# Performance work log

Hardware: AMD Instinct MI355X
Metric: run time of the kernel (lower is better)

Reference implementation:

```python
import jax, jax.numpy as jnp
import numpy as np

N_X, N_U, N_Y = 256, 32, 32
BATCH, T = 16, 8192
LAM_MIN, LAM_MAX = 0.9, 0.995
B_SCALE, D_SCALE = 0.25, 0.25


def setup_inputs() -> dict:
    key = jax.random.key(0)
    k = jax.random.split(key, 6)
    # Orthogonal Q via QR of a random Gaussian matrix (as in the torch module)
    M = jax.random.normal(k[0], (N_X, N_X), dtype=jnp.float32)
    Q, _ = jnp.linalg.qr(M)
    lam = LAM_MIN + (LAM_MAX - LAM_MIN) * jax.random.uniform(k[1], (N_X,), dtype=jnp.float32)
    Bmat = B_SCALE * jax.random.normal(k[2], (N_X, N_U), dtype=jnp.float32)
    # C picks out the first n_y coordinates (C[i, i] = 1)
    C = jnp.eye(N_Y, N_X, dtype=jnp.float32)
    D = D_SCALE * jax.random.normal(k[3], (N_Y, N_U), dtype=jnp.float32)
    x0 = jax.random.normal(k[4], (BATCH, N_X), dtype=jnp.float32)
    u = jax.random.normal(k[5], (BATCH, T, N_U), dtype=jnp.float32)
    return {"x0": x0, "u": u, "Q": Q, "lam": lam, "Bmat": Bmat, "C": C, "D": D}


def _diag_scan(lam, v):
    """Diagonal linear recurrence x_t = lam * x_{t-1} + v_t (x_0 folded into v[:, 0]).

    lam: (N,), v: (B, T, N) -> states x_1..x_T of shape (B, T, N).
    """
    a = jnp.broadcast_to(lam, v.shape)

    def op(l, r):
        a1, b1 = l
        a2, b2 = r
        return a1 * a2, a2 * b1 + b2

    return jax.lax.associative_scan(op, (a, v), axis=1)[1]


def reference(x0, u, Q, lam, Bmat, C, D):
    Bz = Q.T @ Bmat            # (n_x, n_u) modal input matrix
    Cz = C @ Q                 # (n_y, n_x) modal output matrix
    z0 = x0 @ Q                # (B, n_x)   modal initial state
    v = jnp.einsum('btu,nu->btn', u, Bz)   # (B, T, n_x)
    v = v.at[:, 0].add(lam * z0)            # fold lam * z0 into first step
    z_next = _diag_scan(lam, v)             # (B, T, n_x) = z_1..z_T
    # y_t uses z_t for t = 0..T-1 (states[:, :-1] in the original)
    z_prev = jnp.concatenate([z0[:, None, :], z_next[:, :-1]], axis=1)
    y = jnp.einsum('btn,yn->bty', z_prev, Cz) + jnp.einsum('btu,yu->bty', u, D)
    return y
```

## Files before the change

### kernel.cpp

```cpp
#include <hip/hip_runtime.h>

typedef _Float16 half4_t __attribute__((ext_vector_type(4)));
typedef _Float16 half8_t __attribute__((ext_vector_type(8)));
typedef float f32x4 __attribute__((ext_vector_type(4)));

constexpr int NX = 256, NU = 32, NY = 32, BATCH = 16, T = 8192;
constexpr int NC = 64, L = 128;
constexpr int SUBT = 32, NSUB = L / SUBT;
constexpr int KW = NX + NU;
constexpr int ZP = 264;

__global__ __launch_bounds__(256) void k_pre(
    const float* __restrict__ x0, const float* __restrict__ Q,
    const float* __restrict__ Bm, const float* __restrict__ D,
    _Float16* __restrict__ Bzh, _Float16* __restrict__ Wh, float* __restrict__ z0)
{
    int o = blockIdx.x * 64 + (threadIdx.x >> 2);
    int p = threadIdx.x & 3;
    if (o >= 12288) {
        if (p == 0) {
            if (o < 20480) {
                int g = o - 12288; int iy = g >> 8, nn = g & 255;
                Wh[iy * KW + nn] = (_Float16)Q[iy * NX + nn];
            } else if (o < 21504) {
                int g = o - 20480, iy = g >> 5, j = g & 31;
                Wh[iy * KW + NX + j] = (_Float16)D[iy * NU + j];
            }
        }
        return;
    }
    float s = 0.f;
    int k0 = p * 64;
    if (o < 8192) {
        int n = o >> 5, j = o & 31;
        for (int k = k0; k < k0 + 64; ++k) s = fmaf(Q[k * NX + n], Bm[k * NU + j], s);
    } else {
        int g = o - 8192; int b = g >> 8, nn = g & 255;
        for (int k = k0; k < k0 + 64; ++k) s = fmaf(x0[b * NX + k], Q[k * NX + nn], s);
    }
    s += __shfl_xor(s, 1);
    s += __shfl_xor(s, 2);
    if (p == 0) {
        if (o < 8192) Bzh[o] = (_Float16)s;
        else          z0[o - 8192] = s;
    }
}

__global__ __launch_bounds__(256) void k_phase1(
    const float* __restrict__ u, const float* __restrict__ lam,
    const _Float16* __restrict__ Bzh, float* __restrict__ S)
{
    __shared__ __align__(16) _Float16 ut[2][SUBT][32];

    const int b = blockIdx.x >> 6, c = blockIdx.x & 63, tid = threadIdx.x;
    const int w = tid >> 6, lane = tid & 63, m16 = lane & 15, quad = lane >> 4;

    half8_t bfrag[4];
    #pragma unroll
    for (int i = 0; i < 4; ++i)
        bfrag[i] = *(const half8_t*)&Bzh[((4 * w + i) * 16 + m16) * NU + quad * 8];

    float wr[4][4], wt16[4], l32[4], acc[4];
    #pragma unroll
    for (int i = 0; i < 4; ++i) {
        float la = lam[(4 * w + i) * 16 + m16];
        float p2 = la * la, p4 = p2 * p2, p8 = p4 * p4, p16 = p8 * p8;
        float inv1 = 1.0f / la;
        float inv4 = (inv1 * inv1) * (inv1 * inv1);
        float pq = 1.0f;
        if (quad & 1) pq *= inv4;
        if (quad & 2) pq *= inv4 * inv4;
        float w0 = (p16 * p8 * p4 * p2 * la) * pq;
        wr[i][0] = w0;
        wr[i][1] = w0 * inv1;
        wr[i][2] = wr[i][1] * inv1;
        wr[i][3] = wr[i][2] * inv1;
        wt16[i] = 1.0f / p16;
        l32[i] = p16 * p16;
        acc[i] = 0.f;
    }

    const float* ug = u + ((size_t)(b * T) + (size_t)c * L) * NU;

    for (int sub = 0; sub < NSUB; ++sub) {
        {
            float4 uu = *(const float4*)(ug + (size_t)sub * SUBT * NU + tid * 4);
            int tr = tid >> 3, cb = ((tid & 7) * 4 + (tr & 3) * 8) & 31;
            half4_t h; h.x = (_Float16)uu.x; h.y = (_Float16)uu.y;
            h.z = (_Float16)uu.z; h.w = (_Float16)uu.w;
            *(half4_t*)&ut[sub & 1][tr][cb] = h;
        }
        __syncthreads();
        int rot = (m16 & 3) * 8;
        half8_t af0 = *(const half8_t*)&ut[sub & 1][m16][(quad * 8 + rot) & 31];
        half8_t af1 = *(const half8_t*)&ut[sub & 1][16 + m16][(quad * 8 + rot) & 31];
        #pragma unroll
        for (int i = 0; i < 4; ++i) {
            f32x4 z4 = {0.f, 0.f, 0.f, 0.f};
            f32x4 v0 = __builtin_amdgcn_mfma_f32_16x16x32_f16(af0, bfrag[i], z4, 0, 0, 0);
            f32x4 v1 = __builtin_amdgcn_mfma_f32_16x16x32_f16(af1, bfrag[i], z4, 0, 0, 0);
            float s0 = wr[i][0] * v0[0] + wr[i][1] * v0[1] + wr[i][2] * v0[2] + wr[i][3] * v0[3];
            float s1 = wr[i][0] * v1[0] + wr[i][1] * v1[1] + wr[i][2] * v1[2] + wr[i][3] * v1[3];
            acc[i] = fmaf(l32[i], acc[i], fmaf(wt16[i], s1, s0));
        }
    }
    #pragma unroll
    for (int i = 0; i < 4; ++i) {
        acc[i] += __shfl_xor(acc[i], 16);
        acc[i] += __shfl_xor(acc[i], 32);
    }
    float out = quad == 0 ? acc[0] : quad == 1 ? acc[1] : quad == 2 ? acc[2] : acc[3];
    S[(size_t)blockIdx.x * NX + (4 * w + quad) * 16 + m16] = out;
}

__global__ __launch_bounds__(256) void k_phase3(
    const float* __restrict__ u, const float* __restrict__ lam,
    const _Float16* __restrict__ Bzh, const _Float16* __restrict__ Wh,
    const float* __restrict__ S, const float* __restrict__ z0,
    float* __restrict__ y)
{
    __shared__ __align__(16) _Float16 ut[2][SUBT][32];
    __shared__ __align__(16) _Float16 zt[SUBT][ZP];
    __shared__ float pvec[NX];

    const int b = blockIdx.x >> 6, c = blockIdx.x & 63, tid = threadIdx.x;
    const int w = tid >> 6, lane = tid & 63, m16 = lane & 15, quad = lane >> 4;
    const int tw = w & 1, yw = w >> 1;

    {
        float la = lam[tid];
        float l2L = 128.0f * __log2f(la);
        const float* Sb = S + (size_t)(b * NC) * NX + tid;
        float pv = 0.f;
        #pragma unroll 8
        for (int k = 0; k < c; ++k) {
            float wgt = exp2f((float)k * l2L);
            pv = fmaf(wgt, Sb[(size_t)(c - 1 - k) * NX], pv);
        }
        pvec[tid] = fmaf(exp2f((float)c * l2L), z0[b * NX + tid], pv);
    }

    half8_t bfrag[4];
    #pragma unroll
    for (int i = 0; i < 4; ++i)
        bfrag[i] = *(const half8_t*)&Bzh[((4 * w + i) * 16 + m16) * NU + quad * 8];
    half8_t wfrag[9];
    #pragma unroll
    for (int kk = 0; kk < 9; ++kk)
        wfrag[kk] = *(const half8_t*)&Wh[(yw * 16 + m16) * KW + kk * 32 + quad * 8];

    float lamn[4], inv1[4], iq[4], i16p[4], fq[4], f16p[4], l32[4], p[4];
    #pragma unroll
    for (int i = 0; i < 4; ++i) {
        int ni = (4 * w + i) * 16 + m16;
        float la = lam[ni];
        lamn[i] = la;
        float p2 = la * la, p4 = p2 * p2, p8 = p4 * p4, p16 = p8 * p8;
        float iv = 1.0f / la;
        inv1[i] = iv;
        float iv4 = (iv * iv) * (iv * iv);
        float pqi = 1.0f, pqf = 1.0f;
        if (quad & 1) { pqi *= iv4; pqf *= p4; }
        if (quad & 2) { pqi *= iv4 * iv4; pqf *= p8; }
        iq[i] = iv * pqi;
        fq[i] = pqf;
        i16p[i] = 1.0f / p16;
        f16p[i] = p16;
        l32[i] = p16 * p16;
    }
    __syncthreads();
    #pragma unroll
    for (int i = 0; i < 4; ++i)
        p[i] = pvec[(4 * w + i) * 16 + m16];

    const float* ug = u + ((size_t)(b * T) + (size_t)c * L) * NU;
    float* yg = y + ((size_t)(b * T) + (size_t)c * L) * NY;
    const int rot = (m16 & 3) * 8;

    for (int sub = 0; sub < NSUB; ++sub) {
        {
            float4 uu = *(const float4*)(ug + (size_t)sub * SUBT * NU + tid * 4);
            int tr = tid >> 3, cb = ((tid & 7) * 4 + (tr & 3) * 8) & 31;
            half4_t h; h.x = (_Float16)uu.x; h.y = (_Float16)uu.y;
            h.z = (_Float16)uu.z; h.w = (_Float16)uu.w;
            *(half4_t*)&ut[sub & 1][tr][cb] = h;
        }
        __syncthreads();

        half8_t af0 = *(const half8_t*)&ut[sub & 1][m16][(quad * 8 + rot) & 31];
        half8_t af1 = *(const half8_t*)&ut[sub & 1][16 + m16][(quad * 8 + rot) & 31];
        #pragma unroll
        for (int i = 0; i < 4; ++i) {
            int ni = (4 * w + i) * 16 + m16;
            f32x4 z4 = {0.f, 0.f, 0.f, 0.f};
            f32x4 v0 = __builtin_amdgcn_mfma_f32_16x16x32_f16(af0, bfrag[i], z4, 0, 0, 0);
            f32x4 v1 = __builtin_amdgcn_mfma_f32_16x16x32_f16(af1, bfrag[i], z4, 0, 0, 0);
            float a0[4], a1[4];
            float sc = iq[i];
            #pragma unroll
            for (int r = 0; r < 4; ++r) {
                a0[r] = v0[r] * sc;
                a1[r] = v1[r] * (sc * i16p[i]);
                sc *= inv1[i];
            }
            float e0[4], e1[4];
            e0[0] = 0.f; e0[1] = a0[0]; e0[2] = e0[1] + a0[1]; e0[3] = e0[2] + a0[2];
            float S40 = e0[3] + a0[3];
            e1[0] = 0.f; e1[1] = a1[0]; e1[2] = e1[1] + a1[1]; e1[3] = e1[2] + a1[2];
            float S41 = e1[3] + a1[3];
            float incl0 = S40;
            float t0 = __shfl_up(incl0, 16); if (quad >= 1) incl0 += t0;
            t0 = __shfl_up(incl0, 32);       if (quad >= 2) incl0 += t0;
            float excl0 = incl0 - S40;
            float total0 = __shfl(incl0, 48 + m16);
            float incl1 = S41;
            float t1 = __shfl_up(incl1, 16); if (quad >= 1) incl1 += t1;
            t1 = __shfl_up(incl1, 32);       if (quad >= 2) incl1 += t1;
            float excl1 = incl1 - S41;
            float total1 = __shfl(incl1, 48 + m16);
            float f = fq[i];
            #pragma unroll
            for (int r = 0; r < 4; ++r) {
                float zv0 = f * (p[i] + (excl0 + e0[r]));
                float zv1 = (f * f16p[i]) * (p[i] + (total0 + excl1 + e1[r]));
                zt[quad * 4 + r][ni] = (_Float16)zv0;
                zt[16 + quad * 4 + r][ni] = (_Float16)zv1;
                f *= lamn[i];
            }
            p[i] = l32[i] * (p[i] + (total0 + total1));
        }
        __syncthreads();

        f32x4 acc = {0.f, 0.f, 0.f, 0.f};
        #pragma unroll
        for (int kk = 0; kk < 8; ++kk) {
            half8_t az = *(const half8_t*)&zt[tw * 16 + m16][kk * 32 + quad * 8];
            acc = __builtin_amdgcn_mfma_f32_16x16x32_f16(wfrag[kk], az, acc, 0, 0, 0);
        }
        {
            half8_t au = *(const half8_t*)&ut[sub & 1][tw * 16 + m16][(quad * 8 + rot) & 31];
            acc = __builtin_amdgcn_mfma_f32_16x16x32_f16(wfrag[8], au, acc, 0, 0, 0);
        }
        {
            float4 v = make_float4(acc[0], acc[1], acc[2], acc[3]);
            *(float4*)&yg[(size_t)(sub * SUBT + tw * 16 + m16) * NY + yw * 16 + quad * 4] = v;
        }
    }
}

extern "C" void kernel_launch(void* const* d_in, const int* in_sizes, int n_in,
                              void* d_out, int out_size, void* d_ws, size_t ws_size,
                              hipStream_t stream) {
    (void)in_sizes; (void)n_in; (void)out_size; (void)ws_size;
    const float* x0  = (const float*)d_in[0];
    const float* u   = (const float*)d_in[1];
    const float* Q   = (const float*)d_in[2];
    const float* lam = (const float*)d_in[3];
    const float* Bm  = (const float*)d_in[4];
    const float* D   = (const float*)d_in[6];
    float* y = (float*)d_out;

    char* ws = (char*)d_ws;
    _Float16* Bzh = (_Float16*)(ws);
    _Float16* Wh  = (_Float16*)(ws + 16384);
    float*    z0  = (float*)(ws + 34816);
    float*    S   = (float*)(ws + 51200);

    k_pre   <<<336, 256, 0, stream>>>(x0, Q, Bm, D, Bzh, Wh, z0);
    k_phase1<<<BATCH * NC, 256, 0, stream>>>(u, lam, Bzh, S);
    k_phase3<<<BATCH * NC, 256, 0, stream>>>(u, lam, Bzh, Wh, S, z0, y);
}
```

Baseline: 117.1 us.

## Prefetch u tiles in registers, double-buffer z tile, and build W fragments in-kernel

Both phase kernels now load the next u sub-tile into registers two steps ahead and write it to the other shared buffer during compute. This removes the load-then-sync stall at the top of each sub-iteration and saves one barrier per step in phase1. Phase3 double-buffers the z tile so the next step's writes do not conflict with the current MFMA reads, and it reuses the A fragments already in registers for the D term. The Q/D-to-half packing moves out of k_pre into phase3's prologue, which shrinks k_pre, but every phase3 block now re-reads and converts Q and D from global memory. The extra shared memory and registers may lower occupancy.

```diff
diff --git a/kernel.cpp b/kernel.cpp
--- a/kernel.cpp
+++ b/kernel.cpp
@@ -7,28 +7,16 @@
 constexpr int NX = 256, NU = 32, NY = 32, BATCH = 16, T = 8192;
 constexpr int NC = 64, L = 128;
 constexpr int SUBT = 32, NSUB = L / SUBT;
-constexpr int KW = NX + NU;
 constexpr int ZP = 264;
 
 __global__ __launch_bounds__(256) void k_pre(
     const float* __restrict__ x0, const float* __restrict__ Q,
-    const float* __restrict__ Bm, const float* __restrict__ D,
-    _Float16* __restrict__ Bzh, _Float16* __restrict__ Wh, float* __restrict__ z0)
+    const float* __restrict__ Bm,
+    _Float16* __restrict__ Bzh, float* __restrict__ z0)
 {
     int o = blockIdx.x * 64 + (threadIdx.x >> 2);
     int p = threadIdx.x & 3;
-    if (o >= 12288) {
-        if (p == 0) {
-            if (o < 20480) {
-                int g = o - 12288; int iy = g >> 8, nn = g & 255;
-                Wh[iy * KW + nn] = (_Float16)Q[iy * NX + nn];
-            } else if (o < 21504) {
-                int g = o - 20480, iy = g >> 5, j = g & 31;
-                Wh[iy * KW + NX + j] = (_Float16)D[iy * NU + j];
-            }
-        }
-        return;
-    }
+    if (o >= 12288) return;
     float s = 0.f;
     int k0 = p * 64;
     if (o < 8192) {
@@ -54,6 +42,11 @@
 
     const int b = blockIdx.x >> 6, c = blockIdx.x & 63, tid = threadIdx.x;
     const int w = tid >> 6, lane = tid & 63, m16 = lane & 15, quad = lane >> 4;
+    const int rot = (m16 & 3) * 8;
+    const int tr = tid >> 3, cb = ((tid & 7) * 4 + (tr & 3) * 8) & 31;
+
+    const float* ug = u + ((size_t)(b * T) + (size_t)c * L) * NU;
+    float4 ucur = *(const float4*)(ug + tid * 4);
 
     half8_t bfrag[4];
     #pragma unroll
@@ -80,20 +73,19 @@
         acc[i] = 0.f;
     }
 
-    const float* ug = u + ((size_t)(b * T) + (size_t)c * L) * NU;
+    {
+        half4_t h; h.x = (_Float16)ucur.x; h.y = (_Float16)ucur.y;
+        h.z = (_Float16)ucur.z; h.w = (_Float16)ucur.w;
+        *(half4_t*)&ut[0][tr][cb] = h;
+    }
+    __syncthreads();
+    float4 unext = *(const float4*)(ug + (size_t)SUBT * NU + tid * 4);
 
     for (int sub = 0; sub < NSUB; ++sub) {
-        {
-            float4 uu = *(const float4*)(ug + (size_t)sub * SUBT * NU + tid * 4);
-            int tr = tid >> 3, cb = ((tid & 7) * 4 + (tr & 3) * 8) & 31;
-            half4_t h; h.x = (_Float16)uu.x; h.y = (_Float16)uu.y;
-            h.z = (_Float16)uu.z; h.w = (_Float16)uu.w;
-            *(half4_t*)&ut[sub & 1][tr][cb] = h;
-        }
-        __syncthreads();
-        int rot = (m16 & 3) * 8;
         half8_t af0 = *(const half8_t*)&ut[sub & 1][m16][(quad * 8 + rot) & 31];
         half8_t af1 = *(const half8_t*)&ut[sub & 1][16 + m16][(quad * 8 + rot) & 31];
+        if (sub < NSUB - 2)
+            ucur = *(const float4*)(ug + (size_t)(sub + 2) * SUBT * NU + tid * 4);
         #pragma unroll
         for (int i = 0; i < 4; ++i) {
             f32x4 z4 = {0.f, 0.f, 0.f, 0.f};
@@ -103,6 +95,13 @@
             float s1 = wr[i][0] * v1[0] + wr[i][1] * v1[1] + wr[i][2] * v1[2] + wr[i][3] * v1[3];
             acc[i] = fmaf(l32[i], acc[i], fmaf(wt16[i], s1, s0));
         }
+        if (sub < NSUB - 1) {
+            half4_t h; h.x = (_Float16)unext.x; h.y = (_Float16)unext.y;
+            h.z = (_Float16)unext.z; h.w = (_Float16)unext.w;
+            *(half4_t*)&ut[(sub + 1) & 1][tr][cb] = h;
+            unext = ucur;
+            __syncthreads();
+        }
     }
     #pragma unroll
     for (int i = 0; i < 4; ++i) {
@@ -115,17 +114,22 @@
 
 __global__ __launch_bounds__(256) void k_phase3(
     const float* __restrict__ u, const float* __restrict__ lam,
-    const _Float16* __restrict__ Bzh, const _Float16* __restrict__ Wh,
-    const float* __restrict__ S, const float* __restrict__ z0,
-    float* __restrict__ y)
+    const _Float16* __restrict__ Bzh, const float* __restrict__ Q,
+    const float* __restrict__ D, const float* __restrict__ S,
+    const float* __restrict__ z0, float* __restrict__ y)
 {
     __shared__ __align__(16) _Float16 ut[2][SUBT][32];
-    __shared__ __align__(16) _Float16 zt[SUBT][ZP];
+    __shared__ __align__(16) _Float16 zt[2][SUBT][ZP];
     __shared__ float pvec[NX];
 
     const int b = blockIdx.x >> 6, c = blockIdx.x & 63, tid = threadIdx.x;
     const int w = tid >> 6, lane = tid & 63, m16 = lane & 15, quad = lane >> 4;
     const int tw = w & 1, yw = w >> 1;
+    const int rot = (m16 & 3) * 8;
+    const int tr = tid >> 3, cb = ((tid & 7) * 4 + (tr & 3) * 8) & 31;
+
+    const float* ug = u + ((size_t)(b * T) + (size_t)c * L) * NU;
+    float4 ucur = *(const float4*)(ug + tid * 4);
 
     {
         float la = lam[tid];
@@ -146,8 +150,22 @@
         bfrag[i] = *(const half8_t*)&Bzh[((4 * w + i) * 16 + m16) * NU + quad * 8];
     half8_t wfrag[9];
     #pragma unroll
-    for (int kk = 0; kk < 9; ++kk)
-        wfrag[kk] = *(const half8_t*)&Wh[(yw * 16 + m16) * KW + kk * 32 + quad * 8];
+    for (int kk = 0; kk < 8; ++kk) {
+        float4 qa = *(const float4*)&Q[(size_t)(yw * 16 + m16) * NX + kk * 32 + quad * 8];
+        float4 qb = *(const float4*)&Q[(size_t)(yw * 16 + m16) * NX + kk * 32 + quad * 8 + 4];
+        half8_t hh;
+        hh[0] = (_Float16)qa.x; hh[1] = (_Float16)qa.y; hh[2] = (_Float16)qa.z; hh[3] = (_Float16)qa.w;
+        hh[4] = (_Float16)qb.x; hh[5] = (_Float16)qb.y; hh[6] = (_Float16)qb.z; hh[7] = (_Float16)qb.w;
+        wfrag[kk] = hh;
+    }
+    {
+        float4 da = *(const float4*)&D[(size_t)(yw * 16 + m16) * NU + quad * 8];
+        float4 db = *(const float4*)&D[(size_t)(yw * 16 + m16) * NU + quad * 8 + 4];
+        half8_t hh;
+        hh[0] = (_Float16)da.x; hh[1] = (_Float16)da.y; hh[2] = (_Float16)da.z; hh[3] = (_Float16)da.w;
+        hh[4] = (_Float16)db.x; hh[5] = (_Float16)db.y; hh[6] = (_Float16)db.z; hh[7] = (_Float16)db.w;
+        wfrag[8] = hh;
+    }
 
     float lamn[4], inv1[4], iq[4], i16p[4], fq[4], f16p[4], l32[4], p[4];
     #pragma unroll
@@ -168,27 +186,25 @@
         f16p[i] = p16;
         l32[i] = p16 * p16;
     }
+
+    {
+        half4_t h; h.x = (_Float16)ucur.x; h.y = (_Float16)ucur.y;
+        h.z = (_Float16)ucur.z; h.w = (_Float16)ucur.w;
+        *(half4_t*)&ut[0][tr][cb] = h;
+    }
     __syncthreads();
     #pragma unroll
     for (int i = 0; i < 4; ++i)
         p[i] = pvec[(4 * w + i) * 16 + m16];
-
-    const float* ug = u + ((size_t)(b * T) + (size_t)c * L) * NU;
+    float4 unext = *(const float4*)(ug + (size_t)SUBT * NU + tid * 4);
+
     float* yg = y + ((size_t)(b * T) + (size_t)c * L) * NY;
-    const int rot = (m16 & 3) * 8;
 
     for (int sub = 0; sub < NSUB; ++sub) {
-        {
-            float4 uu = *(const float4*)(ug + (size_t)sub * SUBT * NU + tid * 4);
-            int tr = tid >> 3, cb = ((tid & 7) * 4 + (tr & 3) * 8) & 31;
-            half4_t h; h.x = (_Float16)uu.x; h.y = (_Float16)uu.y;
-            h.z = (_Float16)uu.z; h.w = (_Float16)uu.w;
-            *(half4_t*)&ut[sub & 1][tr][cb] = h;
-        }
-        __syncthreads();
-
         half8_t af0 = *(const half8_t*)&ut[sub & 1][m16][(quad * 8 + rot) & 31];
         half8_t af1 = *(const half8_t*)&ut[sub & 1][16 + m16][(quad * 8 + rot) & 31];
+        if (sub < NSUB - 2)
+            ucur = *(const float4*)(ug + (size_t)(sub + 2) * SUBT * NU + tid * 4);
         #pragma unroll
         for (int i = 0; i < 4; ++i) {
             int ni = (4 * w + i) * 16 + m16;
@@ -223,22 +239,28 @@
             for (int r = 0; r < 4; ++r) {
                 float zv0 = f * (p[i] + (excl0 + e0[r]));
                 float zv1 = (f * f16p[i]) * (p[i] + (total0 + excl1 + e1[r]));
-                zt[quad * 4 + r][ni] = (_Float16)zv0;
-                zt[16 + quad * 4 + r][ni] = (_Float16)zv1;
+                zt[sub & 1][quad * 4 + r][ni] = (_Float16)zv0;
+                zt[sub & 1][16 + quad * 4 + r][ni] = (_Float16)zv1;
                 f *= lamn[i];
             }
             p[i] = l32[i] * (p[i] + (total0 + total1));
         }
+        if (sub < NSUB - 1) {
+            half4_t h; h.x = (_Float16)unext.x; h.y = (_Float16)unext.y;
+            h.z = (_Float16)unext.z; h.w = (_Float16)unext.w;
+            *(half4_t*)&ut[(sub + 1) & 1][tr][cb] = h;
+            unext = ucur;
+        }
         __syncthreads();
 
         f32x4 acc = {0.f, 0.f, 0.f, 0.f};
         #pragma unroll
         for (int kk = 0; kk < 8; ++kk) {
-            half8_t az = *(const half8_t*)&zt[tw * 16 + m16][kk * 32 + quad * 8];
+            half8_t az = *(const half8_t*)&zt[sub & 1][tw * 16 + m16][kk * 32 + quad * 8];
             acc = __builtin_amdgcn_mfma_f32_16x16x32_f16(wfrag[kk], az, acc, 0, 0, 0);
         }
         {
-            half8_t au = *(const half8_t*)&ut[sub & 1][tw * 16 + m16][(quad * 8 + rot) & 31];
+            half8_t au = tw ? af1 : af0;
             acc = __builtin_amdgcn_mfma_f32_16x16x32_f16(wfrag[8], au, acc, 0, 0, 0);
         }
         {
@@ -262,11 +284,10 @@
 
     char* ws = (char*)d_ws;
     _Float16* Bzh = (_Float16*)(ws);
-    _Float16* Wh  = (_Float16*)(ws + 16384);
-    float*    z0  = (float*)(ws + 34816);
-    float*    S   = (float*)(ws + 51200);
-
-    k_pre   <<<336, 256, 0, stream>>>(x0, Q, Bm, D, Bzh, Wh, z0);
+    float*    z0  = (float*)(ws + 16384);
+    float*    S   = (float*)(ws + 32768);
+
+    k_pre   <<<192, 256, 0, stream>>>(x0, Q, Bm, Bzh, z0);
     k_phase1<<<BATCH * NC, 256, 0, stream>>>(u, lam, Bzh, S);
-    k_phase3<<<BATCH * NC, 256, 0, stream>>>(u, lam, Bzh, Wh, S, z0, y);
-}
+    k_phase3<<<BATCH * NC, 256, 0, stream>>>(u, lam, Bzh, Q, D, S, z0, y);
+}
```

Result: no change. 118.4 us (+1.1%).
